# Optimization experiments

Hardware: AMD Instinct MI355X
Metric: run time of the kernel (lower is better)

## Reference

```python
import jax, jax.numpy as jnp
import numpy as np
import math

B, S, D, H = 16, 1024, 512, 8
DPH = D // H


def _lorentz_linear(x, W, b, log_scale):
    # LorentzLinear.forward: linear map then project onto hyperboloid
    x = x @ W.T + b
    time = jax.nn.sigmoid(x[..., :1]) * jnp.exp(log_scale) + 1.0 + 1e-4
    rest = x[..., 1:]
    sq = jnp.clip(jnp.sum(rest * rest, axis=-1, keepdims=True), 1e-8, None)
    scale = (time * time - 1.0) / sq
    return jnp.concatenate([time, rest * jnp.sqrt(scale)], axis=-1)


def setup_inputs() -> dict:
    key = jax.random.key(0)
    ks = jax.random.split(key, 16)
    stdv = 1.0 / math.sqrt(D)

    def mk_w(k):
        W = jax.random.uniform(k, (D, D), minval=-stdv, maxval=stdv, dtype=jnp.float32)
        return W.at[:, 0].set(0.0)  # reset_parameters zeroes column 0

    inp = {
        'key': jax.random.normal(ks[0], (B, S, D), dtype=jnp.float32),
        'value': jax.random.normal(ks[1], (B, S, D), dtype=jnp.float32),
        'query': jax.random.normal(ks[2], (B, S, D), dtype=jnp.float32),
        'Wq': mk_w(ks[3]), 'bq': jnp.zeros((D,), jnp.float32), 'lsq': jnp.asarray(math.log(10.0), jnp.float32),
        'Wk': mk_w(ks[4]), 'bk': jnp.zeros((D,), jnp.float32), 'lsk': jnp.asarray(math.log(10.0), jnp.float32),
        'Wv': mk_w(ks[5]), 'bv': jnp.zeros((D,), jnp.float32), 'lsv': jnp.asarray(math.log(10.0), jnp.float32),
        'attn_scale': jnp.asarray([math.sqrt(D)], jnp.float32),
        'attn_bias': jnp.zeros((), jnp.float32),
    }
    return inp


def reference(key, value, query, Wq, bq, lsq, Wk, bk, lsk, Wv, bv, lsv, attn_scale, attn_bias):
    q = _lorentz_linear(query, Wq, bq, lsq)  # [B,S,D]
    k = _lorentz_linear(key, Wk, bk, lsk)
    v = _lorentz_linear(value, Wv, bv, lsv)

    def shape(x):
        b, s, _ = x.shape
        return x.reshape(b, s, H, DPH).transpose(0, 2, 1, 3)  # [B,H,S,dph]

    q, k, v = shape(q), shape(k), shape(v)

    # Minkowski signature (-,+,...,+) on the per-head feature dim
    sgn = jnp.concatenate([-jnp.ones((1,), q.dtype), jnp.ones((DPH - 1,), q.dtype)])

    # attn = (2 + 2 * cinner(q, k)) / scale + bias  (no softmax, per source)
    attn = (2.0 + 2.0 * jnp.einsum('bhqd,bhkd->bhqk', q * sgn, k)) / attn_scale + attn_bias

    # mid_point: ave = attn @ v, then normalize by sqrt(|<ave,ave>_L|)
    ave = jnp.einsum('bhqk,bhkd->bhqd', attn, v)
    inner = jnp.sum(ave * ave * sgn, axis=-1, keepdims=True)  # Lorentz inner product
    denom = jnp.sqrt(jnp.clip(jnp.abs(inner), 1e-8, None))
    ctx = ave / denom  # [B,H,S,dph]

    b = ctx.shape[0]
    return ctx.transpose(0, 2, 1, 3).reshape(b, -1, H * DPH)  # [B,S,D]
```

## Files before the change

kernel.cpp:

```cpp
#include <hip/hip_runtime.h>
#include <stdint.h>

#define B_    16
#define S_    1024
#define D_    512
#define H_    8
#define DPH_  64
#define MTOT  (B_*S_)

typedef __attribute__((ext_vector_type(8))) short  short8;
typedef __attribute__((ext_vector_type(4))) float  float4v;
typedef __attribute__((ext_vector_type(4))) ushort u16x4;

__device__ inline float bf2f(ushort u) {
    union { uint32_t u; float f; } c; c.u = ((uint32_t)u) << 16; return c.f;
}
__device__ inline ushort f2bf(float f) {
    union { float f; uint32_t u; } c; c.f = f;
    uint32_t x = c.u;
    return (ushort)((x + 0x7fffu + ((x >> 16) & 1u)) >> 16);
}
__device__ inline bool mode_f32(const void* as) {
    return ((const ushort*)as)[0] == (ushort)0x04F3u;
}

typedef __attribute__((address_space(1))) uint32_t glob_u32;
typedef __attribute__((address_space(3))) uint32_t lds_u32;
__device__ __forceinline__ void gload16(const ushort* g, ushort* l) {
    __builtin_amdgcn_global_load_lds((glob_u32*)g, (lds_u32*)l, 16, 0, 0);
}

__global__ __launch_bounds__(256) void gemm_proj(
    const void* __restrict__ Xq, const void* __restrict__ Xk, const void* __restrict__ Xv,
    const void* __restrict__ Wq, const void* __restrict__ Wk, const void* __restrict__ Wv,
    const void* __restrict__ bq, const void* __restrict__ bk, const void* __restrict__ bv,
    const void* __restrict__ as_flag,
    float* __restrict__ Yq, float* __restrict__ Yk, float* __restrict__ Yv,
    float* __restrict__ RowY0, float* __restrict__ RowSq)
{
    const int z = blockIdx.z;
    const void* X    = z == 0 ? Xq : (z == 1 ? Xk : Xv);
    const void* W    = z == 0 ? Wq : (z == 1 ? Wk : Wv);
    const void* bias = z == 0 ? bq : (z == 1 ? bk : bv);
    float*      Y    = z == 0 ? Yq : (z == 1 ? Yk : Yv);
    const bool  f32  = mode_f32(as_flag);

    const int m0   = blockIdx.x * 128;
    const int n0   = blockIdx.y * 128;
    const int tid  = threadIdx.x;
    const int lane = tid & 63;
    const int w    = tid >> 6;
    const int wm   = w >> 1, wn = w & 1;

    __shared__ __align__(16) char smem[32768];
    ushort* s16 = (ushort*)smem;

    float4v acc[4][4];
    #pragma unroll
    for (int i = 0; i < 4; ++i)
        #pragma unroll
        for (int j = 0; j < 4; ++j)
            acc[i][j] = (float4v){0.f, 0.f, 0.f, 0.f};

    const int fr = lane & 15;
    const int fk = (lane >> 4) * 8;
    int offA[4], offB[4];
    #pragma unroll
    for (int i = 0; i < 4; ++i) offA[i] = (wm * 64 + i * 16 + fr) * 32 + fk;
    #pragma unroll
    for (int j = 0; j < 4; ++j) offB[j] = (wn * 64 + j * 16 + fr) * 32 + fk;

    if (!f32) {
        const ushort* Xu = (const ushort*)X;
        const ushort* Wu = (const ushort*)W;
        const int rsub = lane >> 2;
        const int cg   = (lane & 3) * 8;
        const ushort* gA0 = Xu + (size_t)(m0 + w * 16      + rsub) * D_ + cg;
        const ushort* gA1 = Xu + (size_t)(m0 + w * 16 + 64 + rsub) * D_ + cg;
        const ushort* gB0 = Wu + (size_t)(n0 + w * 16      + rsub) * D_ + cg;
        const ushort* gB1 = Wu + (size_t)(n0 + w * 16 + 64 + rsub) * D_ + cg;
        const int dA0 = w * 512;
        const int dA1 = 2048 + w * 512;

        gload16(gA0, &s16[dA0]);
        gload16(gA1, &s16[dA1]);
        gload16(gB0, &s16[4096 + dA0]);
        gload16(gB1, &s16[4096 + dA1]);
        __syncthreads();

        int cur = 0;
        for (int kt = 32; kt < D_; kt += 32) {
            const int nb = (cur ^ 1) * 8192;
            gload16(gA0 + kt, &s16[nb + dA0]);
            gload16(gA1 + kt, &s16[nb + dA1]);
            gload16(gB0 + kt, &s16[nb + 4096 + dA0]);
            gload16(gB1 + kt, &s16[nb + 4096 + dA1]);
            const ushort* bb = &s16[cur * 8192];
            short8 ah[4], bh[4];
            #pragma unroll
            for (int i = 0; i < 4; ++i) ah[i] = *(const short8*)&bb[offA[i]];
            #pragma unroll
            for (int j = 0; j < 4; ++j) bh[j] = *(const short8*)&bb[4096 + offB[j]];
            #pragma unroll
            for (int i = 0; i < 4; ++i)
                #pragma unroll
                for (int j = 0; j < 4; ++j)
                    acc[i][j] = __builtin_amdgcn_mfma_f32_16x16x32_bf16(ah[i], bh[j], acc[i][j], 0, 0, 0);
            __syncthreads();
            cur ^= 1;
        }
        {
            const ushort* bb = &s16[cur * 8192];
            short8 ah[4], bh[4];
            #pragma unroll
            for (int i = 0; i < 4; ++i) ah[i] = *(const short8*)&bb[offA[i]];
            #pragma unroll
            for (int j = 0; j < 4; ++j) bh[j] = *(const short8*)&bb[4096 + offB[j]];
            #pragma unroll
            for (int i = 0; i < 4; ++i)
                #pragma unroll
                for (int j = 0; j < 4; ++j)
                    acc[i][j] = __builtin_amdgcn_mfma_f32_16x16x32_bf16(ah[i], bh[j], acc[i][j], 0, 0, 0);
        }
    } else {
        const float* Xf = (const float*)X;
        const float* Wf = (const float*)W;
        for (int kt = 0; kt < D_; kt += 32) {
            __syncthreads();
            u16x4 rbl[4];
            #pragma unroll
            for (int it = 0; it < 4; ++it) {
                const int c = tid + it * 256;
                const int row = c >> 3, c4 = (c & 7) * 4;
                const float4 fa = *(const float4*)&Xf[(size_t)(m0 + row) * D_ + kt + c4];
                const float4 fb = *(const float4*)&Wf[(size_t)(n0 + row) * D_ + kt + c4];
                u16x4 ah4, al4, bh4;
                #pragma unroll
                for (int q = 0; q < 4; ++q) {
                    const float fav = (&fa.x)[q], fbv = (&fb.x)[q];
                    const ushort ha = f2bf(fav), hb = f2bf(fbv);
                    ah4[q] = ha; al4[q] = f2bf(fav - bf2f(ha));
                    bh4[q] = hb; rbl[it][q] = f2bf(fbv - bf2f(hb));
                }
                *(u16x4*)&s16[row * 32 + c4]        = ah4;
                *(u16x4*)&s16[4096 + row * 32 + c4] = al4;
                *(u16x4*)&s16[8192 + row * 32 + c4] = bh4;
            }
            __syncthreads();
            short8 ah[4], al[4], bx[4];
            #pragma unroll
            for (int i = 0; i < 4; ++i) {
                ah[i] = *(const short8*)&s16[offA[i]];
                al[i] = *(const short8*)&s16[4096 + offA[i]];
            }
            #pragma unroll
            for (int j = 0; j < 4; ++j) bx[j] = *(const short8*)&s16[8192 + offB[j]];
            #pragma unroll
            for (int i = 0; i < 4; ++i)
                #pragma unroll
                for (int j = 0; j < 4; ++j) {
                    acc[i][j] = __builtin_amdgcn_mfma_f32_16x16x32_bf16(ah[i], bx[j], acc[i][j], 0, 0, 0);
                    acc[i][j] = __builtin_amdgcn_mfma_f32_16x16x32_bf16(al[i], bx[j], acc[i][j], 0, 0, 0);
                }
            __syncthreads();
            #pragma unroll
            for (int it = 0; it < 4; ++it) {
                const int c = tid + it * 256;
                const int row = c >> 3, c4 = (c & 7) * 4;
                *(u16x4*)&s16[8192 + row * 32 + c4] = rbl[it];
            }
            __syncthreads();
            #pragma unroll
            for (int j = 0; j < 4; ++j) bx[j] = *(const short8*)&s16[8192 + offB[j]];
            #pragma unroll
            for (int i = 0; i < 4; ++i)
                #pragma unroll
                for (int j = 0; j < 4; ++j)
                    acc[i][j] = __builtin_amdgcn_mfma_f32_16x16x32_bf16(ah[i], bx[j], acc[i][j], 0, 0, 0);
        }
    }

    __syncthreads();
    float* sRS = (float*)smem;
    const int er = lane >> 4;
    float bvf[4];
    #pragma unroll
    for (int j = 0; j < 4; ++j) {
        const int n = n0 + wn * 64 + j * 16 + fr;
        bvf[j] = f32 ? ((const float*)bias)[n] : bf2f(((const ushort*)bias)[n]);
    }
    #pragma unroll
    for (int i = 0; i < 4; ++i)
        #pragma unroll
        for (int r = 0; r < 4; ++r) {
            const int row = wm * 64 + i * 16 + er * 4 + r;
            const int m = m0 + row;
            float rsum = 0.f;
            #pragma unroll
            for (int j = 0; j < 4; ++j) {
                const int n = n0 + wn * 64 + j * 16 + fr;
                const float y = acc[i][j][r] + bvf[j];
                Y[(size_t)m * D_ + n] = y;
                if (n != 0) rsum += y * y;
            }
            rsum += __shfl_xor(rsum, 1, 64);
            rsum += __shfl_xor(rsum, 2, 64);
            rsum += __shfl_xor(rsum, 4, 64);
            rsum += __shfl_xor(rsum, 8, 64);
            if (fr == 0) sRS[wn * 128 + row] = rsum;
            if (blockIdx.y == 0 && wn == 0 && fr == 0)
                RowY0[z * MTOT + m] = acc[i][0][r] + bvf[0];
        }
    __syncthreads();
    if (tid < 128) {
        const float v = sRS[tid] + sRS[128 + tid];
        atomicAdd(&RowSq[z * MTOT + m0 + tid], v);
    }
}

__global__ __launch_bounds__(256) void rowfix(
    float* __restrict__ T, float* __restrict__ A,
    const void* __restrict__ lq, const void* __restrict__ lk, const void* __restrict__ lv,
    const void* __restrict__ as_flag)
{
    const int idx = blockIdx.x * 256 + threadIdx.x;
    const int z = idx >> 14;
    const bool f32 = mode_f32(as_flag);
    const void* lsp = z == 0 ? lq : (z == 1 ? lk : lv);
    const float ls = f32 ? ((const float*)lsp)[0] : bf2f(((const ushort*)lsp)[0]);
    const float y0 = T[idx];
    const float sq = fmaxf(A[idx], 1e-8f);
    const float t = (1.f / (1.f + expf(-y0))) * expf(ls) + 1.0f + 1e-4f;
    T[idx] = t;
    A[idx] = sqrtf((t * t - 1.0f) / sq);
}

__global__ __launch_bounds__(256) void kv_k(
    const float* __restrict__ Yk, const float* __restrict__ Yv,
    const float* __restrict__ T, const float* __restrict__ A,
    float* __restrict__ KV, float* __restrict__ Vs)
{
    const int bh = blockIdx.x;
    const int sp = blockIdx.y;
    const int b = bh >> 3, h = bh & 7;
    const int t = threadIdx.x;
    const int td = t & 15, te = t >> 4;

    __shared__ float sK[16][64];
    __shared__ float sV[16][64];

    float acc[4][4] = {};
    float vs[4] = {0.f, 0.f, 0.f, 0.f};

    const int r  = t >> 4;
    const int c4 = (t & 15) * 4;
    const size_t mbase = (size_t)b * S_ + (size_t)sp * 128;

    for (int sc = 0; sc < 128; sc += 16) {
        const size_t m = mbase + sc + r;
        __syncthreads();
        float4 kr = *(const float4*)&Yk[m * D_ + h * DPH_ + c4];
        float4 vr = *(const float4*)&Yv[m * D_ + h * DPH_ + c4];
        const float ak = A[MTOT + m],     tk = T[MTOT + m];
        const float av = A[2 * MTOT + m], tv = T[2 * MTOT + m];
        kr.x *= ak; kr.y *= ak; kr.z *= ak; kr.w *= ak;
        vr.x *= av; vr.y *= av; vr.z *= av; vr.w *= av;
        if (h == 0 && c4 == 0) { kr.x = tk; vr.x = tv; }
        *(float4*)&sK[r][c4] = kr;
        *(float4*)&sV[r][c4] = vr;
        __syncthreads();
        #pragma unroll
        for (int rr = 0; rr < 16; ++rr) {
            const float4 k4 = *(const float4*)&sK[rr][te * 4];
            const float4 v4 = *(const float4*)&sV[rr][td * 4];
            #pragma unroll
            for (int i = 0; i < 4; ++i)
                #pragma unroll
                for (int j = 0; j < 4; ++j)
                    acc[i][j] += (&k4.x)[i] * (&v4.x)[j];
            #pragma unroll
            for (int j = 0; j < 4; ++j) vs[j] += (&v4.x)[j];
        }
    }

    #pragma unroll
    for (int i = 0; i < 4; ++i)
        #pragma unroll
        for (int j = 0; j < 4; ++j)
            atomicAdd(&KV[(size_t)bh * 4096 + (te * 4 + i) * 64 + td * 4 + j],
                      acc[i][j]);
    if (te == 0) {
        #pragma unroll
        for (int j = 0; j < 4; ++j)
            atomicAdd(&Vs[(size_t)bh * 64 + td * 4 + j], vs[j]);
    }
}

__global__ __launch_bounds__(256) void ave_norm(
    const float* __restrict__ Yq, const float* __restrict__ T, const float* __restrict__ A,
    const float* __restrict__ KV, const float* __restrict__ Vs,
    const void* __restrict__ as_ptr, const void* __restrict__ ab_ptr,
    void* __restrict__ outp)
{
    const int bh = blockIdx.x >> 3;
    const int st = blockIdx.x & 7;
    const int b = bh >> 3, h = bh & 7;
    const int s0 = st * 128;
    const int t = threadIdx.x;
    const int lane = t & 63;
    const int w = t >> 6;
    const bool f32 = mode_f32(as_ptr);

    __shared__ ushort sKVh[64 * 64];
    __shared__ ushort sKVl[64 * 64];
    __shared__ ushort sQh[128 * 64];
    __shared__ ushort sQl[128 * 64];
    __shared__ float  sVs[64];

    #pragma unroll
    for (int i = 0; i < 16; ++i) {
        const int idx = t + i * 256;
        const int e = idx >> 6, d = idx & 63;
        const float v = KV[(size_t)bh * 4096 + idx];
        const ushort hi = f2bf(v);
        sKVh[d * 64 + e] = hi;
        sKVl[d * 64 + e] = f2bf(v - bf2f(hi));
    }
    if (t < 64) sVs[t] = Vs[(size_t)bh * 64 + t];
    #pragma unroll
    for (int i = 0; i < 8; ++i) {
        const int idx = t + i * 256;
        const int row = idx >> 4, c4 = (idx & 15) * 4;
        const size_t m = (size_t)b * S_ + s0 + row;
        const float4 q4 = *(const float4*)&Yq[m * D_ + h * DPH_ + c4];
        const float alpha = A[m], tim = T[m];
        #pragma unroll
        for (int q = 0; q < 4; ++q) {
            const int col = c4 + q;
            float val = (&q4.x)[q] * alpha;
            if (h == 0 && col == 0) val = tim;
            if (col == 0) val = -val;
            const ushort hi = f2bf(val);
            sQh[row * 64 + col] = hi;
            sQl[row * 64 + col] = f2bf(val - bf2f(hi));
        }
    }
    __syncthreads();

    const float asv = f32 ? ((const float*)as_ptr)[0] : bf2f(((const ushort*)as_ptr)[0]);
    const float abv = f32 ? ((const float*)ab_ptr)[0] : bf2f(((const ushort*)ab_ptr)[0]);
    const float c1f = 2.0f / asv;
    const float c0f = c1f + abv;

    const int fr = lane & 15, fq = lane >> 4;

    float4v acc[2][4];
    #pragma unroll
    for (int mi = 0; mi < 2; ++mi)
        #pragma unroll
        for (int j = 0; j < 4; ++j)
            acc[mi][j] = (float4v){0.f, 0.f, 0.f, 0.f};

    #pragma unroll
    for (int kk = 0; kk < 2; ++kk) {
        const int ko = kk * 32 + fq * 8;
        short8 ah[2], al[2], bh4[4], bl4[4];
        #pragma unroll
        for (int mi = 0; mi < 2; ++mi) {
            ah[mi] = *(const short8*)&sQh[(w * 32 + mi * 16 + fr) * 64 + ko];
            al[mi] = *(const short8*)&sQl[(w * 32 + mi * 16 + fr) * 64 + ko];
        }
        #pragma unroll
        for (int j = 0; j < 4; ++j) {
            bh4[j] = *(const short8*)&sKVh[(j * 16 + fr) * 64 + ko];
            bl4[j] = *(const short8*)&sKVl[(j * 16 + fr) * 64 + ko];
        }
        #pragma unroll
        for (int mi = 0; mi < 2; ++mi)
            #pragma unroll
            for (int j = 0; j < 4; ++j) {
                acc[mi][j] = __builtin_amdgcn_mfma_f32_16x16x32_bf16(ah[mi], bh4[j], acc[mi][j], 0, 0, 0);
                acc[mi][j] = __builtin_amdgcn_mfma_f32_16x16x32_bf16(ah[mi], bl4[j], acc[mi][j], 0, 0, 0);
                acc[mi][j] = __builtin_amdgcn_mfma_f32_16x16x32_bf16(al[mi], bh4[j], acc[mi][j], 0, 0, 0);
            }
    }

    #pragma unroll
    for (int mi = 0; mi < 2; ++mi) {
        float avev[4][4];
        float part[4] = {0.f, 0.f, 0.f, 0.f};
        #pragma unroll
        for (int j = 0; j < 4; ++j) {
            const float vsn = sVs[j * 16 + fr];
            #pragma unroll
            for (int r = 0; r < 4; ++r) {
                const float a = c1f * acc[mi][j][r] + c0f * vsn;
                avev[j][r] = a;
                part[r] += (j == 0 && fr == 0) ? -(a * a) : (a * a);
            }
        }
        #pragma unroll
        for (int off = 1; off < 16; off <<= 1)
            #pragma unroll
            for (int r = 0; r < 4; ++r)
                part[r] += __shfl_xor(part[r], off, 64);
        float rd[4];
        #pragma unroll
        for (int r = 0; r < 4; ++r)
            rd[r] = 1.0f / sqrtf(fmaxf(fabsf(part[r]), 1e-8f));
        #pragma unroll
        for (int j = 0; j < 4; ++j)
            #pragma unroll
            for (int r = 0; r < 4; ++r) {
                const int srow = s0 + w * 32 + mi * 16 + fq * 4 + r;
                const size_t oidx = ((size_t)b * S_ + srow) * D_ + h * DPH_ + j * 16 + fr;
                const float cv = avev[j][r] * rd[r];
                if (f32) ((float*)outp)[oidx] = cv;
                else     ((ushort*)outp)[oidx] = f2bf(cv);
            }
    }
}

extern "C" void kernel_launch(void* const* d_in, const int* in_sizes, int n_in,
                              void* d_out, int out_size, void* d_ws, size_t ws_size,
                              hipStream_t stream)
{
    const void* key    = d_in[0];
    const void* value  = d_in[1];
    const void* query  = d_in[2];
    const void* Wq     = d_in[3];
    const void* bq     = d_in[4];
    const void* lsq    = d_in[5];
    const void* Wk     = d_in[6];
    const void* bk     = d_in[7];
    const void* lsk    = d_in[8];
    const void* Wv     = d_in[9];
    const void* bv     = d_in[10];
    const void* lsv    = d_in[11];
    const void* ascale = d_in[12];
    const void* abias  = d_in[13];

    char* ws = (char*)d_ws;
    float* Yq    = (float*)(ws + 0);
    float* Yk    = (float*)(ws + 33554432);
    float* Yv    = (float*)(ws + 67108864);
    float* T     = (float*)(ws + 100663296);
    float* Alpha = (float*)(ws + 100859904);
    float* KV    = (float*)(ws + 101056512);
    float* Vs    = (float*)(ws + 103153664);

    hipMemsetAsync(ws + 100859904, 0, 2326528, stream);

    gemm_proj<<<dim3(MTOT / 128, D_ / 128, 3), 256, 0, stream>>>(
        query, key, value, Wq, Wk, Wv, bq, bk, bv, ascale,
        Yq, Yk, Yv, T, Alpha);
    rowfix<<<(3 * MTOT) / 256, 256, 0, stream>>>(T, Alpha, lsq, lsk, lsv, ascale);
    kv_k<<<dim3(B_ * H_, 8), 256, 0, stream>>>(Yk, Yv, T, Alpha, KV, Vs);
    ave_norm<<<B_ * H_ * (S_ / 128), 256, 0, stream>>>(
        Yq, T, Alpha, KV, Vs, ascale, abias, d_out);
}
```

Before: 341.9 us.

## Prefetch next f32 tile into registers, swizzle LDS, store B-low split once

In the fp32 projection GEMM path, the next K-tile's global loads are issued before the MFMA block and converted to bf16 hi/lo pairs afterward, so load latency overlaps compute. All four split planes (A hi/lo, B hi/lo) now live in LDS together, which removes the extra sync and rewrite pass for B-low. The LDS layout is also XOR-style swizzled to reduce bank conflicts. The cost is more registers held across the loop, which may reduce occupancy.

```diff
diff --git a/kernel.cpp b/kernel.cpp
--- a/kernel.cpp
+++ b/kernel.cpp
@@ -64,13 +64,13 @@
 
     const int fr = lane & 15;
     const int fk = (lane >> 4) * 8;
-    int offA[4], offB[4];
-    #pragma unroll
-    for (int i = 0; i < 4; ++i) offA[i] = (wm * 64 + i * 16 + fr) * 32 + fk;
-    #pragma unroll
-    for (int j = 0; j < 4; ++j) offB[j] = (wn * 64 + j * 16 + fr) * 32 + fk;
 
     if (!f32) {
+        int offA[4], offB[4];
+        #pragma unroll
+        for (int i = 0; i < 4; ++i) offA[i] = (wm * 64 + i * 16 + fr) * 32 + fk;
+        #pragma unroll
+        for (int j = 0; j < 4; ++j) offB[j] = (wn * 64 + j * 16 + fr) * 32 + fk;
         const ushort* Xu = (const ushort*)X;
         const ushort* Wu = (const ushort*)W;
         const int rsub = lane >> 2;
@@ -125,58 +125,91 @@
     } else {
         const float* Xf = (const float*)X;
         const float* Wf = (const float*)W;
+
+        int wrow[4], wc4[4], woff[4];
+        #pragma unroll
+        for (int it = 0; it < 4; ++it) {
+            const int c = tid + it * 256;
+            const int row = c >> 3, c4 = (c & 7) * 4;
+            wrow[it] = row; wc4[it] = c4;
+            woff[it] = row * 32 + ((((c4 >> 3) + (row >> 1)) & 3) << 3) + (c4 & 4);
+        }
+        int offAs[4], offBs[4];
+        #pragma unroll
+        for (int i = 0; i < 4; ++i) {
+            const int row = wm * 64 + i * 16 + fr;
+            offAs[i] = row * 32 + ((((fk >> 3) + (row >> 1)) & 3) << 3);
+        }
+        #pragma unroll
+        for (int j = 0; j < 4; ++j) {
+            const int row = wn * 64 + j * 16 + fr;
+            offBs[j] = row * 32 + ((((fk >> 3) + (row >> 1)) & 3) << 3);
+        }
+
+        float4 fa[4], fb[4];
+        u16x4 wah[4], wal[4], wbh[4], wbl[4];
+
+        #pragma unroll
+        for (int it = 0; it < 4; ++it) {
+            fa[it] = *(const float4*)&Xf[(size_t)(m0 + wrow[it]) * D_ + wc4[it]];
+            fb[it] = *(const float4*)&Wf[(size_t)(n0 + wrow[it]) * D_ + wc4[it]];
+        }
+        #pragma unroll
+        for (int it = 0; it < 4; ++it)
+            #pragma unroll
+            for (int q = 0; q < 4; ++q) {
+                const float fav = (&fa[it].x)[q], fbv = (&fb[it].x)[q];
+                const ushort ha = f2bf(fav), hb = f2bf(fbv);
+                wah[it][q] = ha; wal[it][q] = f2bf(fav - bf2f(ha));
+                wbh[it][q] = hb; wbl[it][q] = f2bf(fbv - bf2f(hb));
+            }
+
         for (int kt = 0; kt < D_; kt += 32) {
+            if (kt) __syncthreads();
+            #pragma unroll
+            for (int it = 0; it < 4; ++it) {
+                *(u16x4*)&s16[woff[it]]          = wah[it];
+                *(u16x4*)&s16[4096  + woff[it]]  = wal[it];
+                *(u16x4*)&s16[8192  + woff[it]]  = wbh[it];
+                *(u16x4*)&s16[12288 + woff[it]]  = wbl[it];
+            }
+            const bool more = (kt + 32 < D_);
+            if (more) {
+                #pragma unroll
+                for (int it = 0; it < 4; ++it) {
+                    fa[it] = *(const float4*)&Xf[(size_t)(m0 + wrow[it]) * D_ + kt + 32 + wc4[it]];
+                    fb[it] = *(const float4*)&Wf[(size_t)(n0 + wrow[it]) * D_ + kt + 32 + wc4[it]];
+                }
+            }
             __syncthreads();
-            u16x4 rbl[4];
-            #pragma unroll
-            for (int it = 0; it < 4; ++it) {
-                const int c = tid + it * 256;
-                const int row = c >> 3, c4 = (c & 7) * 4;
-                const float4 fa = *(const float4*)&Xf[(size_t)(m0 + row) * D_ + kt + c4];
-                const float4 fb = *(const float4*)&Wf[(size_t)(n0 + row) * D_ + kt + c4];
-                u16x4 ah4, al4, bh4;
-                #pragma unroll
-                for (int q = 0; q < 4; ++q) {
-                    const float fav = (&fa.x)[q], fbv = (&fb.x)[q];
-                    const ushort ha = f2bf(fav), hb = f2bf(fbv);
-                    ah4[q] = ha; al4[q] = f2bf(fav - bf2f(ha));
-                    bh4[q] = hb; rbl[it][q] = f2bf(fbv - bf2f(hb));
+            short8 ah[4], al[4];
+            #pragma unroll
+            for (int i = 0; i < 4; ++i) {
+                ah[i] = *(const short8*)&s16[offAs[i]];
+                al[i] = *(const short8*)&s16[4096 + offAs[i]];
+            }
+            #pragma unroll
+            for (int j = 0; j < 4; ++j) {
+                const short8 bh = *(const short8*)&s16[8192  + offBs[j]];
+                const short8 bl = *(const short8*)&s16[12288 + offBs[j]];
+                #pragma unroll
+                for (int i = 0; i < 4; ++i) {
+                    acc[i][j] = __builtin_amdgcn_mfma_f32_16x16x32_bf16(ah[i], bh, acc[i][j], 0, 0, 0);
+                    acc[i][j] = __builtin_amdgcn_mfma_f32_16x16x32_bf16(al[i], bh, acc[i][j], 0, 0, 0);
+                    acc[i][j] = __builtin_amdgcn_mfma_f32_16x16x32_bf16(ah[i], bl, acc[i][j], 0, 0, 0);
                 }
-                *(u16x4*)&s16[row * 32 + c4]        = ah4;
-                *(u16x4*)&s16[4096 + row * 32 + c4] = al4;
-                *(u16x4*)&s16[8192 + row * 32 + c4] = bh4;
-            }
-            __syncthreads();
-            short8 ah[4], al[4], bx[4];
-            #pragma unroll
-            for (int i = 0; i < 4; ++i) {
-                ah[i] = *(const short8*)&s16[offA[i]];
-                al[i] = *(const short8*)&s16[4096 + offA[i]];
-            }
-            #pragma unroll
-            for (int j = 0; j < 4; ++j) bx[j] = *(const short8*)&s16[8192 + offB[j]];
-            #pragma unroll
-            for (int i = 0; i < 4; ++i)
-                #pragma unroll
-                for (int j = 0; j < 4; ++j) {
-                    acc[i][j] = __builtin_amdgcn_mfma_f32_16x16x32_bf16(ah[i], bx[j], acc[i][j], 0, 0, 0);
-                    acc[i][j] = __builtin_amdgcn_mfma_f32_16x16x32_bf16(al[i], bx[j], acc[i][j], 0, 0, 0);
-                }
-            __syncthreads();
-            #pragma unroll
-            for (int it = 0; it < 4; ++it) {
-                const int c = tid + it * 256;
-                const int row = c >> 3, c4 = (c & 7) * 4;
-                *(u16x4*)&s16[8192 + row * 32 + c4] = rbl[it];
-            }
-            __syncthreads();
-            #pragma unroll
-            for (int j = 0; j < 4; ++j) bx[j] = *(const short8*)&s16[8192 + offB[j]];
-            #pragma unroll
-            for (int i = 0; i < 4; ++i)
-                #pragma unroll
-                for (int j = 0; j < 4; ++j)
-                    acc[i][j] = __builtin_amdgcn_mfma_f32_16x16x32_bf16(ah[i], bx[j], acc[i][j], 0, 0, 0);
+            }
+            if (more) {
+                #pragma unroll
+                for (int it = 0; it < 4; ++it)
+                    #pragma unroll
+                    for (int q = 0; q < 4; ++q) {
+                        const float fav = (&fa[it].x)[q], fbv = (&fb[it].x)[q];
+                        const ushort ha = f2bf(fav), hb = f2bf(fbv);
+                        wah[it][q] = ha; wal[it][q] = f2bf(fav - bf2f(ha));
+                        wbh[it][q] = hb; wbl[it][q] = f2bf(fbv - bf2f(hb));
+                    }
+            }
         }
     }
 
```

Measured after the change: 398.1 us. +16.4%, slower.
